# Kernel optimization log

Hardware: AMD Instinct MI355X
Metric: run time of the kernel (lower is better)

Reference implementation:

```python
import jax, jax.numpy as jnp
import numpy as np

N, LQ, C = 1, 12240, 256
HEADS, LEVELS, FRAMES, POINTS = 8, 4, 4, 4
D_HEAD = C // HEADS  # 32
SHAPES = np.array([[48, 48, 4], [24, 24, 4], [12, 12, 4], [6, 6, 4]], np.int32)  # (H, W, T)
LEN_IN = int((SHAPES[:, 0] * SHAPES[:, 1] * SHAPES[:, 2]).sum())  # 12240
assert LEN_IN == LQ


def setup_inputs() -> dict:
    key = jax.random.key(0)
    ks = jax.random.split(key, 9)
    starts = np.concatenate([[0], np.cumsum(SHAPES[:, 0] * SHAPES[:, 1] * SHAPES[:, 2])[:-1]]).astype(np.int32)
    off_dim = HEADS * LEVELS * FRAMES * POINTS * 2
    attn_dim = HEADS * LEVELS * FRAMES * POINTS
    s = 1.0 / np.sqrt(C)
    return {
        "query": jax.random.normal(ks[0], (N, LQ, C), jnp.float32),
        "reference_points": jax.random.uniform(ks[1], (N, LQ, LEVELS, 2), dtype=jnp.float32),
        "temporal_offsets": 0.05 * jax.random.normal(ks[2], (LQ, LEVELS, FRAMES, 2), jnp.float32),
        "input_flatten": jax.random.normal(ks[3], (N, LEN_IN, C), jnp.float32),
        "input_spatial_shapes": jnp.asarray(SHAPES),
        "input_level_start_index": jnp.asarray(starts),
        "W_off": 0.01 * jax.random.normal(ks[4], (C, off_dim), jnp.float32),
        "b_off": 0.1 * jax.random.normal(ks[5], (off_dim,), jnp.float32),
        "W_attn": 0.02 * jax.random.normal(ks[6], (C, attn_dim), jnp.float32),
        "b_attn": jnp.zeros((attn_dim,), jnp.float32),
        "W_val": s * jax.random.normal(ks[7], (C, C), jnp.float32),
        "b_val": jnp.zeros((C,), jnp.float32),
        "W_out": s * jax.random.normal(ks[8], (C, C), jnp.float32),
        "b_out": jnp.zeros((C,), jnp.float32),
    }


def ms_deform_core(value, shapes_hw, starts, loc, attn_w):
    """value: (N, Len_in, Hh, D); loc: (N, Lq, Hh, L, P, 2) in [0,1];
    attn_w: (N, Lq, Hh, L, P); shapes_hw/starts: python ints per level.
    Bilinear sampling matches F.grid_sample(align_corners=False, padding_mode='zeros')."""
    n, _, hh, d = value.shape
    lq, p = loc.shape[1], loc.shape[4]
    out = jnp.zeros((n, hh, lq, d), value.dtype)
    for lid, (hl, wl) in enumerate(shapes_hw):
        s0 = starts[lid]
        v = jnp.transpose(value[:, s0:s0 + hl * wl], (0, 2, 1, 3))  # (N, Hh, H*W, D)
        x = loc[:, :, :, lid, :, 0] * wl - 0.5  # (N, Lq, Hh, P) pixel coords
        y = loc[:, :, :, lid, :, 1] * hl - 0.5
        x0 = jnp.floor(x)
        y0 = jnp.floor(y)
        fx, fy = x - x0, y - y0
        x0i, y0i = x0.astype(jnp.int32), y0.astype(jnp.int32)
        acc = jnp.zeros((n, hh, lq, p, d), value.dtype)
        corners = ((0, 0, (1 - fx) * (1 - fy)), (0, 1, fx * (1 - fy)),
                   (1, 0, (1 - fx) * fy), (1, 1, fx * fy))
        for dy, dx, w in corners:
            xi, yi = x0i + dx, y0i + dy
            valid = (xi >= 0) & (xi < wl) & (yi >= 0) & (yi < hl)
            idx = jnp.clip(yi, 0, hl - 1) * wl + jnp.clip(xi, 0, wl - 1)  # (N, Lq, Hh, P)
            idx_t = jnp.transpose(idx, (0, 2, 1, 3)).reshape(n, hh, lq * p, 1)
            g = jnp.take_along_axis(v, idx_t, axis=2).reshape(n, hh, lq, p, d)
            wm = jnp.transpose(jnp.where(valid, w, 0.0), (0, 2, 1, 3))  # (N, Hh, Lq, P)
            acc = acc + g * wm[..., None]
        aw = jnp.transpose(attn_w[:, :, :, lid], (0, 2, 1, 3))  # (N, Hh, Lq, P)
        out = out + jnp.sum(acc * aw[..., None], axis=3)
    return jnp.transpose(out, (0, 2, 1, 3)).reshape(n, lq, hh * d)


def reference(query, reference_points, temporal_offsets, input_flatten,
              input_spatial_shapes, input_level_start_index,
              W_off, b_off, W_attn, b_attn, W_val, b_val, W_out, b_out):
    shapes = np.asarray(input_spatial_shapes)  # static (L, 3) = (H, W, T)
    starts = [int(s) for s in np.asarray(input_level_start_index)]
    n, lq, _ = query.shape
    value = (input_flatten @ W_val + b_val).reshape(n, -1, HEADS, D_HEAD)
    attn = jax.nn.softmax((query @ W_attn + b_attn)
                          .reshape(n, lq, HEADS, LEVELS * FRAMES * POINTS), axis=-1)
    attn = attn.reshape(n, lq, HEADS, LEVELS, FRAMES * POINTS)
    off = (query @ W_off + b_off).reshape(n, lq, HEADS, LEVELS, FRAMES, POINTS, 2)
    # offset_normalizer = (T, H*W) per level: x spans frames, y spans flattened pixels
    norm = jnp.stack([jnp.asarray(shapes[:, 2], jnp.float32),
                      jnp.asarray(shapes[:, 0] * shapes[:, 1], jnp.float32)], axis=-1)  # (L, 2)
    loc = temporal_offsets[None, :, None, :, :, None, :] + off / norm[None, None, None, :, None, None, :]
    loc = loc.reshape(n, lq, HEADS, LEVELS, FRAMES * POINTS, 2)
    loc = reference_points[:, :, None, :, None, :] + loc
    shapes_hw = [(int(h) * int(w), int(t)) for h, w, t in shapes]  # (H*W, T) grids
    out = ms_deform_core(value, shapes_hw, starts, loc, attn)
    return out @ W_out + b_out
```

## Files before the change

kernel.cpp:

```cpp
#include <hip/hip_runtime.h>
#include <hip/hip_bf16.h>
#include <hip/hip_fp16.h>

#define LQ     12240

typedef _Float16 half8 __attribute__((ext_vector_type(8)));
typedef float floatx4 __attribute__((ext_vector_type(4)));
typedef unsigned int uint;

__global__ __launch_bounds__(256) void cvt_f32_f16(
    const float* __restrict__ in, __half* __restrict__ out, int n4) {
  const int i = blockIdx.x * 256 + threadIdx.x;
  if (i >= n4) return;
  const float4 v = reinterpret_cast<const float4*>(in)[i];
  const __half2 a = __floats2half2_rn(v.x, v.y);
  const __half2 b = __floats2half2_rn(v.z, v.w);
  uint2 pk;
  pk.x = *reinterpret_cast<const uint*>(&a);
  pk.y = *reinterpret_cast<const uint*>(&b);
  reinterpret_cast<uint2*>(out)[i] = pk;
}

__global__ __launch_bounds__(256) void transpose_cvt(
    const float* __restrict__ in, __half* __restrict__ out, int N) {
  __shared__ float t[32][33];
  const int n0 = blockIdx.x * 32, k0 = blockIdx.y * 32;
  const int c = threadIdx.x & 31, r = threadIdx.x >> 5;
#pragma unroll
  for (int i = 0; i < 4; ++i)
    t[r + i * 8][c] = in[(size_t)(k0 + r + i * 8) * N + n0 + c];
  __syncthreads();
#pragma unroll
  for (int i = 0; i < 4; ++i)
    out[(size_t)(n0 + r + i * 8) * 256 + k0 + c] = __float2half(t[c][r + i * 8]);
}

template <typename TC>
__device__ inline void store_c(TC* C, size_t idx, float v);
template <> __device__ inline void store_c<float>(float* C, size_t idx, float v) { C[idx] = v; }
template <> __device__ inline void store_c<__half>(__half* C, size_t idx, float v) { C[idx] = __float2half(v); }

template <typename TC>
__global__ __launch_bounds__(256) void gemm_mfma(
    const __half* __restrict__ A,
    const __half* __restrict__ Bt,
    const float* __restrict__ bias,
    TC* __restrict__ C, int M, int N) {
  __shared__ uint4 As_g[128 * 8];
  __shared__ uint4 Bs_g[128 * 8];

  const int tid = threadIdx.x;
  const int bm = blockIdx.y * 128, bn = blockIdx.x * 128;
  const int wid = tid >> 6, lane = tid & 63;
  const int wr = wid >> 1, wn = wid & 1;
  const int l16 = lane & 15, lhi = lane >> 4;

  floatx4 acc[4][4] = {};

  const int srow = tid >> 1;
  const int sg0 = (tid & 1) * 4;
  const bool arow_ok = (bm + srow) < M;
  const __half* Arow = A + (size_t)(arow_ok ? bm + srow : 0) * 256;
  const __half* Brow = Bt + (size_t)(bn + srow) * 256;

  for (int ks = 0; ks < 4; ++ks) {
    const int k0 = ks * 64;
#pragma unroll
    for (int i = 0; i < 4; ++i) {
      const int g = sg0 + i;
      uint4 av = make_uint4(0, 0, 0, 0);
      if (arow_ok) av = *reinterpret_cast<const uint4*>(Arow + k0 + g * 8);
      As_g[srow * 8 + (g ^ (srow & 7))] = av;
      Bs_g[srow * 8 + (g ^ (srow & 7))] =
          *reinterpret_cast<const uint4*>(Brow + k0 + g * 8);
    }
    __syncthreads();

#pragma unroll
    for (int kk = 0; kk < 2; ++kk) {
      half8 a[4], b[4];
#pragma unroll
      for (int m = 0; m < 4; ++m) {
        const int row = wr * 64 + m * 16 + l16;
        const int g = kk * 4 + lhi;
        union { uint4 u; half8 h; } cv;
        cv.u = As_g[row * 8 + (g ^ (row & 7))];
        a[m] = cv.h;
      }
#pragma unroll
      for (int n = 0; n < 4; ++n) {
        const int row = wn * 64 + n * 16 + l16;
        const int g = kk * 4 + lhi;
        union { uint4 u; half8 h; } cv;
        cv.u = Bs_g[row * 8 + (g ^ (row & 7))];
        b[n] = cv.h;
      }
#pragma unroll
      for (int m = 0; m < 4; ++m)
#pragma unroll
        for (int n = 0; n < 4; ++n)
          acc[m][n] = __builtin_amdgcn_mfma_f32_16x16x32_f16(a[m], b[n], acc[m][n], 0, 0, 0);
    }
    __syncthreads();
  }

#pragma unroll
  for (int m = 0; m < 4; ++m) {
    const int row0 = bm + wr * 64 + m * 16 + lhi * 4;
#pragma unroll
    for (int n = 0; n < 4; ++n) {
      const int col = bn + wn * 64 + n * 16 + l16;
      const float bv = bias[col];
#pragma unroll
      for (int r = 0; r < 4; ++r) {
        const int row = row0 + r;
        if (row < M) store_c<TC>(C, (size_t)row * N + col, acc[m][n][r] + bv);
      }
    }
  }
}

__device__ inline uint hfma2u(uint a, uint b, uint c) {
  const __half2 ah = *reinterpret_cast<const __half2*>(&a);
  const __half2 bh = *reinterpret_cast<const __half2*>(&b);
  const __half2 ch = *reinterpret_cast<const __half2*>(&c);
  const __half2 r = __hfma2(ah, bh, ch);
  return *reinterpret_cast<const uint*>(&r);
}

__device__ inline uint pack_wr(float w, uint row) {
  const __half hw = __float2half(w);
  return ((uint)__half_as_ushort(hw) << 16) | row;
}

__global__ __launch_bounds__(256, 8) void sample_kernel(
    const __half* __restrict__ value,
    const __half* __restrict__ logits,
    const __half* __restrict__ off,
    const float* __restrict__ tempoff,
    const float* __restrict__ refpts,
    __half* __restrict__ msout) {
  const int q0 = blockIdx.x * 2;
  const int tid = threadIdx.x;

  __shared__ __align__(16) uint spk[4096];
  float* slog = reinterpret_cast<float*>(spk);
  __shared__ float sm_m[16], sm_si[16];

#pragma unroll
  for (int k = 0; k < 4; ++k) {
    const int s = tid + k * 256;
    slog[s] = __half2float(logits[(size_t)(q0 + (s >> 9)) * 512 + (s & 511)]);
  }
  __syncthreads();

  {
    const int g = tid >> 4;
    const int j = tid & 15;
    const float* e = &slog[g * 64];
    float m = fmaxf(fmaxf(e[j], e[j + 16]), fmaxf(e[j + 32], e[j + 48]));
#pragma unroll
    for (int mask = 8; mask >= 1; mask >>= 1) m = fmaxf(m, __shfl_xor(m, mask));
    float s = __expf(e[j] - m) + __expf(e[j + 16] - m) +
              __expf(e[j + 32] - m) + __expf(e[j + 48] - m);
#pragma unroll
    for (int mask = 8; mask >= 1; mask >>= 1) s += __shfl_xor(s, mask);
    if (j == 0) { sm_m[g] = m; sm_si[g] = 1.0f / s; }
  }
  __syncthreads();

  const float HWF[4] = {2304.f, 576.f, 144.f, 36.f};
  const float RHW[4] = {1.f / 2304.f, 1.f / 576.f, 1.f / 144.f, 1.f / 36.f};
  const int   S0[4]  = {0, 9216, 11520, 12096};
  const int   HWI[4] = {2304, 576, 144, 36};

  uint4 rec[4];
  int   ridx[4];
  const int h1   = tid & 7;
  const int smid = (tid >> 3) & 7;
  const int shi  = (tid >> 6) & 3;

#pragma unroll
  for (int k = 0; k < 4; ++k) {
    const int qi = k & 1;
    const int s  = smid | (shi << 3) | ((k >> 1) << 5);
    const int i  = h1 * 64 + s;
    const int l  = s >> 4;
    const int f  = (s >> 2) & 3;
    const size_t q = (size_t)(q0 + qi);
    const int g = (qi << 3) | h1;

    const float w = __expf(slog[(qi << 9) + i] - sm_m[g]) * sm_si[g];

    const float2 o  = __half22float2(*reinterpret_cast<const __half2*>(&off[q * 1024 + i * 2]));
    const float2 to = *reinterpret_cast<const float2*>(&tempoff[q * 32 + (l * 4 + f) * 2]);
    const float2 rp = *reinterpret_cast<const float2*>(&refpts[q * 8 + l * 2]);

    const float hw = HWF[l];
    const float x = (to.x + o.x * 0.25f + rp.x) * 4.0f - 0.5f;
    const float y = (to.y + o.y * RHW[l] + rp.y) * hw - 0.5f;

    const float x0f = floorf(x), y0f = floorf(y);
    const float fx = x - x0f, fy = y - y0f;
    const int x0 = (int)x0f, y0 = (int)y0f;
    const int hl = HWI[l];

    const bool xv0 = (x0 >= 0) && (x0 < 4);
    const bool xv1 = (x0 >= -1) && (x0 < 3);
    const bool yv0 = (y0 >= 0) && (y0 < hl);
    const bool yv1 = (y0 >= -1) && (y0 < hl - 1);
    const int xc0 = min(max(x0, 0), 3);
    const int xc1 = min(max(x0 + 1, 0), 3);
    const int yc0 = min(max(y0, 0), hl - 1);
    const int yc1 = min(max(y0 + 1, 0), hl - 1);

    const float w00 = (xv0 && yv0) ? w * (1.f - fx) * (1.f - fy) : 0.f;
    const float w01 = (xv1 && yv0) ? w * fx * (1.f - fy) : 0.f;
    const float w10 = (xv0 && yv1) ? w * (1.f - fx) * fy : 0.f;
    const float w11 = (xv1 && yv1) ? w * fx * fy : 0.f;

    const int base = S0[l];
    rec[k] = make_uint4(pack_wr(w00, (uint)(base + yc0 * 4 + xc0)),
                        pack_wr(w01, (uint)(base + yc0 * 4 + xc1)),
                        pack_wr(w10, (uint)(base + yc1 * 4 + xc0)),
                        pack_wr(w11, (uint)(base + yc1 * 4 + xc1)));
    ridx[k] = (qi << 9) | (s << 3) | h1;
  }
  __syncthreads();

  uint4* spk4 = reinterpret_cast<uint4*>(spk);
#pragma unroll
  for (int k = 0; k < 4; ++k) spk4[ridx[k]] = rec[k];
  __syncthreads();

  const int qi = tid >> 7;
  const int h  = (tid >> 4) & 7;
  const int c  = (tid >> 2) & 3;
  const int d  = tid & 3;

  const uint* __restrict__ sp = spk + ((qi << 11) | (h << 2) | c);
  const char* __restrict__ vbase = (const char*)value + h * 64 + d * 16;

  float f0 = 0.f, f1 = 0.f, f2 = 0.f, f3 = 0.f;
  float f4 = 0.f, f5 = 0.f, f6 = 0.f, f7 = 0.f;

#pragma unroll
  for (int l = 0; l < 4; ++l) {
    uint a0 = 0u, a1 = 0u, a2 = 0u, a3 = 0u;
#pragma unroll
    for (int t = 0; t < 16; ++t) {
      const uint pk = sp[(l * 16 + t) << 5];
      const uint wdup = __builtin_amdgcn_perm(pk, pk, 0x03020302u);
      const uint4 v = *reinterpret_cast<const uint4*>(vbase + ((pk & 0xFFFFu) << 9));
      a0 = hfma2u(wdup, v.x, a0);
      a1 = hfma2u(wdup, v.y, a1);
      a2 = hfma2u(wdup, v.z, a2);
      a3 = hfma2u(wdup, v.w, a3);
    }
    const float2 p0 = __half22float2(*reinterpret_cast<const __half2*>(&a0));
    const float2 p1 = __half22float2(*reinterpret_cast<const __half2*>(&a1));
    const float2 p2 = __half22float2(*reinterpret_cast<const __half2*>(&a2));
    const float2 p3 = __half22float2(*reinterpret_cast<const __half2*>(&a3));
    f0 += p0.x; f1 += p0.y; f2 += p1.x; f3 += p1.y;
    f4 += p2.x; f5 += p2.y; f6 += p3.x; f7 += p3.y;
  }

#pragma unroll
  for (int mask = 4; mask <= 8; mask <<= 1) {
    f0 += __shfl_xor(f0, mask); f1 += __shfl_xor(f1, mask);
    f2 += __shfl_xor(f2, mask); f3 += __shfl_xor(f3, mask);
    f4 += __shfl_xor(f4, mask); f5 += __shfl_xor(f5, mask);
    f6 += __shfl_xor(f6, mask); f7 += __shfl_xor(f7, mask);
  }

  if (c == 0) {
    const __half2 o0 = __floats2half2_rn(f0, f1);
    const __half2 o1 = __floats2half2_rn(f2, f3);
    const __half2 o2 = __floats2half2_rn(f4, f5);
    const __half2 o3 = __floats2half2_rn(f6, f7);
    uint4 st;
    st.x = *reinterpret_cast<const uint*>(&o0);
    st.y = *reinterpret_cast<const uint*>(&o1);
    st.z = *reinterpret_cast<const uint*>(&o2);
    st.w = *reinterpret_cast<const uint*>(&o3);
    *reinterpret_cast<uint4*>(&msout[(size_t)(q0 + qi) * 256 + h * 32 + d * 8]) = st;
  }
}

extern "C" void kernel_launch(void* const* d_in, const int* in_sizes, int n_in,
                              void* d_out, int out_size, void* d_ws, size_t ws_size,
                              hipStream_t stream) {
  const float* query   = (const float*)d_in[0];
  const float* refpts  = (const float*)d_in[1];
  const float* tempoff = (const float*)d_in[2];
  const float* inflat  = (const float*)d_in[3];
  const float* W_off  = (const float*)d_in[6];
  const float* b_off  = (const float*)d_in[7];
  const float* W_attn = (const float*)d_in[8];
  const float* b_attn = (const float*)d_in[9];
  const float* W_val  = (const float*)d_in[10];
  const float* b_val  = (const float*)d_in[11];
  const float* W_out  = (const float*)d_in[12];
  const float* b_out  = (const float*)d_in[13];

  char* ws = (char*)d_ws;
  const size_t szQ = (size_t)LQ * 256 * 2;
  __half* qh     = (__half*)ws;                 ws += szQ;
  __half* ifh    = (__half*)ws;                 ws += szQ;
  __half* wT_val = (__half*)ws;                 ws += (size_t)256 * 256 * 2;
  __half* wT_att = (__half*)ws;                 ws += (size_t)512 * 256 * 2;
  __half* wT_off = (__half*)ws;                 ws += (size_t)1024 * 256 * 2;
  __half* wT_out = (__half*)ws;                 ws += (size_t)256 * 256 * 2;
  __half* val_h  = (__half*)ws;                 ws += szQ;
  __half* attn_h = (__half*)ws;                 ws += (size_t)LQ * 512 * 2;
  __half* off_h  = (__half*)ws;                 ws += (size_t)LQ * 1024 * 2;
  __half* ms_h   = (__half*)ws;                 ws += szQ;

  const dim3 blk(256);
  const int n4 = LQ * 256 / 4;

  cvt_f32_f16<<<dim3((n4 + 255) / 256), blk, 0, stream>>>(query, qh, n4);
  cvt_f32_f16<<<dim3((n4 + 255) / 256), blk, 0, stream>>>(inflat, ifh, n4);
  transpose_cvt<<<dim3(8, 8),  blk, 0, stream>>>(W_val,  wT_val, 256);
  transpose_cvt<<<dim3(16, 8), blk, 0, stream>>>(W_attn, wT_att, 512);
  transpose_cvt<<<dim3(32, 8), blk, 0, stream>>>(W_off,  wT_off, 1024);
  transpose_cvt<<<dim3(8, 8),  blk, 0, stream>>>(W_out,  wT_out, 256);

  const int gm = (LQ + 127) / 128;
  gemm_mfma<__half><<<dim3(2, gm), blk, 0, stream>>>(ifh, wT_val, b_val, val_h, LQ, 256);
  gemm_mfma<__half><<<dim3(4, gm), blk, 0, stream>>>(qh, wT_att, b_attn, attn_h, LQ, 512);
  gemm_mfma<__half><<<dim3(8, gm), blk, 0, stream>>>(qh, wT_off, b_off, off_h, LQ, 1024);

  sample_kernel<<<dim3(LQ / 2), blk, 0, stream>>>(val_h, attn_h, off_h, tempoff, refpts, ms_h);

  gemm_mfma<float><<<dim3(2, gm), blk, 0, stream>>>(ms_h, wT_out, b_out, (float*)d_out, LQ, 256);
}
```

Baseline: 144.3 us.

## Merge prep and projection launches and load GEMM tiles via global_load_lds

The two fp32-to-fp16 conversions become one launch, and the four weight transposes become one launch. The value, attention and offset projection GEMMs merge into a single grid, with the attention and offset weights concatenated into one 1536-wide output that the sampler reads at new offsets. GEMM tile loads now go straight from global memory to LDS with global_load_lds, using a vmcnt wait and scheduling barriers. The aim is to cut launch count and the register round-trip on tile staging. The trade-off is a wider strided output buffer, and the loads are still not double-buffered.

```diff
diff --git a/kernel.cpp b/kernel.cpp
--- a/kernel.cpp
+++ b/kernel.cpp
@@ -8,23 +8,39 @@
 typedef float floatx4 __attribute__((ext_vector_type(4)));
 typedef unsigned int uint;
 
-__global__ __launch_bounds__(256) void cvt_f32_f16(
-    const float* __restrict__ in, __half* __restrict__ out, int n4) {
-  const int i = blockIdx.x * 256 + threadIdx.x;
-  if (i >= n4) return;
+__global__ __launch_bounds__(256) void cvt2_f32_f16(
+    const float* __restrict__ a, const float* __restrict__ b,
+    __half* __restrict__ oa, __half* __restrict__ ob, int n4each) {
+  int i = blockIdx.x * 256 + threadIdx.x;
+  const float* in = a;
+  __half* out = oa;
+  if (i >= n4each) { in = b; out = ob; i -= n4each; }
   const float4 v = reinterpret_cast<const float4*>(in)[i];
-  const __half2 a = __floats2half2_rn(v.x, v.y);
-  const __half2 b = __floats2half2_rn(v.z, v.w);
+  const __half2 p0 = __floats2half2_rn(v.x, v.y);
+  const __half2 p1 = __floats2half2_rn(v.z, v.w);
   uint2 pk;
-  pk.x = *reinterpret_cast<const uint*>(&a);
-  pk.y = *reinterpret_cast<const uint*>(&b);
+  pk.x = *reinterpret_cast<const uint*>(&p0);
+  pk.y = *reinterpret_cast<const uint*>(&p1);
   reinterpret_cast<uint2*>(out)[i] = pk;
 }
 
-__global__ __launch_bounds__(256) void transpose_cvt(
-    const float* __restrict__ in, __half* __restrict__ out, int N) {
+__global__ __launch_bounds__(256) void transpose_all(
+    const float* __restrict__ W_val, const float* __restrict__ W_attn,
+    const float* __restrict__ W_off, const float* __restrict__ W_out,
+    __half* __restrict__ wT_val, __half* __restrict__ wT_ao,
+    __half* __restrict__ wT_out) {
+  int b = blockIdx.x;
+  const float* in;
+  __half* out;
+  int N;
+  if (b < 64) { in = W_val; out = wT_val; N = 256; }
+  else if (b < 192) { b -= 64; in = W_attn; out = wT_ao; N = 512; }
+  else if (b < 448) { b -= 192; in = W_off; out = wT_ao + (size_t)512 * 256; N = 1024; }
+  else { b -= 448; in = W_out; out = wT_out; N = 256; }
+  const int nb = N / 32;
+  const int n0 = (b % nb) * 32, k0 = (b / nb) * 32;
+
   __shared__ float t[32][33];
-  const int n0 = blockIdx.x * 32, k0 = blockIdx.y * 32;
   const int c = threadIdx.x & 31, r = threadIdx.x >> 5;
 #pragma unroll
   for (int i = 0; i < 4; ++i)
@@ -33,6 +49,12 @@
 #pragma unroll
   for (int i = 0; i < 4; ++i)
     out[(size_t)(n0 + r + i * 8) * 256 + k0 + c] = __float2half(t[c][r + i * 8]);
+}
+
+__device__ inline void gl_lds16(const __half* g, void* lds) {
+  __builtin_amdgcn_global_load_lds(
+      (const __attribute__((address_space(1))) void*)g,
+      (__attribute__((address_space(3))) void*)lds, 16, 0, 0);
 }
 
 template <typename TC>
@@ -41,39 +63,40 @@
 template <> __device__ inline void store_c<__half>(__half* C, size_t idx, float v) { C[idx] = __float2half(v); }
 
 template <typename TC>
-__global__ __launch_bounds__(256) void gemm_mfma(
-    const __half* __restrict__ A,
-    const __half* __restrict__ Bt,
-    const float* __restrict__ bias,
-    TC* __restrict__ C, int M, int N) {
-  __shared__ uint4 As_g[128 * 8];
-  __shared__ uint4 Bs_g[128 * 8];
+__device__ inline void gemm_core(
+    const __half* __restrict__ A, const __half* __restrict__ Bt,
+    const float* __restrict__ bias, int coff, TC* __restrict__ C,
+    int M, int N, int bm, int bn) {
+  __shared__ uint4 As_g[1024];
+  __shared__ uint4 Bs_g[1024];
 
   const int tid = threadIdx.x;
-  const int bm = blockIdx.y * 128, bn = blockIdx.x * 128;
-  const int wid = tid >> 6, lane = tid & 63;
-  const int wr = wid >> 1, wn = wid & 1;
+  const int w = tid >> 6, lane = tid & 63;
+  const int wr = w >> 1, wn = w & 1;
   const int l16 = lane & 15, lhi = lane >> 4;
 
   floatx4 acc[4][4] = {};
 
-  const int srow = tid >> 1;
-  const int sg0 = (tid & 1) * 4;
-  const bool arow_ok = (bm + srow) < M;
-  const __half* Arow = A + (size_t)(arow_ok ? bm + srow : 0) * 256;
-  const __half* Brow = Bt + (size_t)(bn + srow) * 256;
+  int srow[4], sgr[4];
+#pragma unroll
+  for (int j = 0; j < 4; ++j) {
+    const int idx = (w * 4 + j) * 64 + lane;
+    srow[j] = idx >> 3;
+    sgr[j] = (idx & 7) ^ (srow[j] & 7);
+  }
 
   for (int ks = 0; ks < 4; ++ks) {
     const int k0 = ks * 64;
 #pragma unroll
-    for (int i = 0; i < 4; ++i) {
-      const int g = sg0 + i;
-      uint4 av = make_uint4(0, 0, 0, 0);
-      if (arow_ok) av = *reinterpret_cast<const uint4*>(Arow + k0 + g * 8);
-      As_g[srow * 8 + (g ^ (srow & 7))] = av;
-      Bs_g[srow * 8 + (g ^ (srow & 7))] =
-          *reinterpret_cast<const uint4*>(Brow + k0 + g * 8);
+    for (int j = 0; j < 4; ++j) {
+      int ar = bm + srow[j];
+      if (ar >= M) ar = M - 1;
+      gl_lds16(A + (size_t)ar * 256 + k0 + sgr[j] * 8, &As_g[(w * 4 + j) * 64]);
+      gl_lds16(Bt + (size_t)(bn + srow[j]) * 256 + k0 + sgr[j] * 8,
+               &Bs_g[(w * 4 + j) * 64]);
     }
+    asm volatile("s_waitcnt vmcnt(0)" ::: "memory");
+    __builtin_amdgcn_sched_barrier(0);
     __syncthreads();
 
 #pragma unroll
@@ -101,7 +124,9 @@
         for (int n = 0; n < 4; ++n)
           acc[m][n] = __builtin_amdgcn_mfma_f32_16x16x32_f16(a[m], b[n], acc[m][n], 0, 0, 0);
     }
+    __builtin_amdgcn_sched_barrier(0);
     __syncthreads();
+    __builtin_amdgcn_sched_barrier(0);
   }
 
 #pragma unroll
@@ -110,7 +135,7 @@
 #pragma unroll
     for (int n = 0; n < 4; ++n) {
       const int col = bn + wn * 64 + n * 16 + l16;
-      const float bv = bias[col];
+      const float bv = bias[col - coff];
 #pragma unroll
       for (int r = 0; r < 4; ++r) {
         const int row = row0 + r;
@@ -118,6 +143,31 @@
       }
     }
   }
+}
+
+__global__ __launch_bounds__(256) void gemm_fused(
+    const __half* __restrict__ qh, const __half* __restrict__ ifh,
+    const __half* __restrict__ wT_val, const __half* __restrict__ wT_ao,
+    const float* __restrict__ b_val, const float* __restrict__ b_attn,
+    const float* __restrict__ b_off,
+    __half* __restrict__ val_h, __half* __restrict__ ao_h, int M) {
+  const int bx = blockIdx.x;
+  const int bm = blockIdx.y * 128;
+  if (bx < 2) {
+    gemm_core<__half>(ifh, wT_val, b_val, 0, val_h, M, 256, bm, bx * 128);
+  } else {
+    const int bn = (bx - 2) * 128;
+    const float* bias = (bn < 512) ? b_attn : b_off;
+    const int coff = (bn < 512) ? 0 : 512;
+    gemm_core<__half>(qh, wT_ao, bias, coff, ao_h, M, 1536, bm, bn);
+  }
+}
+
+__global__ __launch_bounds__(256) void gemm_out_k(
+    const __half* __restrict__ ms_h, const __half* __restrict__ wT_out,
+    const float* __restrict__ b_out, float* __restrict__ C, int M) {
+  gemm_core<float>(ms_h, wT_out, b_out, 0, C, M, 256, blockIdx.y * 128,
+                   blockIdx.x * 128);
 }
 
 __device__ inline uint hfma2u(uint a, uint b, uint c) {
@@ -135,8 +185,7 @@
 
 __global__ __launch_bounds__(256, 8) void sample_kernel(
     const __half* __restrict__ value,
-    const __half* __restrict__ logits,
-    const __half* __restrict__ off,
+    const __half* __restrict__ ao,
     const float* __restrict__ tempoff,
     const float* __restrict__ refpts,
     __half* __restrict__ msout) {
@@ -150,7 +199,7 @@
 #pragma unroll
   for (int k = 0; k < 4; ++k) {
     const int s = tid + k * 256;
-    slog[s] = __half2float(logits[(size_t)(q0 + (s >> 9)) * 512 + (s & 511)]);
+    slog[s] = __half2float(ao[(size_t)(q0 + (s >> 9)) * 1536 + (s & 511)]);
   }
   __syncthreads();
 
@@ -192,7 +241,7 @@
 
     const float w = __expf(slog[(qi << 9) + i] - sm_m[g]) * sm_si[g];
 
-    const float2 o  = __half22float2(*reinterpret_cast<const __half2*>(&off[q * 1024 + i * 2]));
+    const float2 o  = __half22float2(*reinterpret_cast<const __half2*>(&ao[q * 1536 + 512 + i * 2]));
     const float2 to = *reinterpret_cast<const float2*>(&tempoff[q * 32 + (l * 4 + f) * 2]);
     const float2 rp = *reinterpret_cast<const float2*>(&refpts[q * 8 + l * 2]);
 
@@ -308,30 +357,25 @@
   __half* qh     = (__half*)ws;                 ws += szQ;
   __half* ifh    = (__half*)ws;                 ws += szQ;
   __half* wT_val = (__half*)ws;                 ws += (size_t)256 * 256 * 2;
-  __half* wT_att = (__half*)ws;                 ws += (size_t)512 * 256 * 2;
-  __half* wT_off = (__half*)ws;                 ws += (size_t)1024 * 256 * 2;
+  __half* wT_ao  = (__half*)ws;                 ws += (size_t)1536 * 256 * 2;
   __half* wT_out = (__half*)ws;                 ws += (size_t)256 * 256 * 2;
   __half* val_h  = (__half*)ws;                 ws += szQ;
-  __half* attn_h = (__half*)ws;                 ws += (size_t)LQ * 512 * 2;
-  __half* off_h  = (__half*)ws;                 ws += (size_t)LQ * 1024 * 2;
+  __half* ao_h   = (__half*)ws;                 ws += (size_t)LQ * 1536 * 2;
   __half* ms_h   = (__half*)ws;                 ws += szQ;
 
   const dim3 blk(256);
-  const int n4 = LQ * 256 / 4;
-
-  cvt_f32_f16<<<dim3((n4 + 255) / 256), blk, 0, stream>>>(query, qh, n4);
-  cvt_f32_f16<<<dim3((n4 + 255) / 256), blk, 0, stream>>>(inflat, ifh, n4);
-  transpose_cvt<<<dim3(8, 8),  blk, 0, stream>>>(W_val,  wT_val, 256);
-  transpose_cvt<<<dim3(16, 8), blk, 0, stream>>>(W_attn, wT_att, 512);
-  transpose_cvt<<<dim3(32, 8), blk, 0, stream>>>(W_off,  wT_off, 1024);
-  transpose_cvt<<<dim3(8, 8),  blk, 0, stream>>>(W_out,  wT_out, 256);
+  const int n4each = LQ * 256 / 4;
+
+  cvt2_f32_f16<<<dim3(2 * n4each / 256), blk, 0, stream>>>(query, inflat, qh, ifh, n4each);
+  transpose_all<<<dim3(512), blk, 0, stream>>>(W_val, W_attn, W_off, W_out,
+                                               wT_val, wT_ao, wT_out);
 
   const int gm = (LQ + 127) / 128;
-  gemm_mfma<__half><<<dim3(2, gm), blk, 0, stream>>>(ifh, wT_val, b_val, val_h, LQ, 256);
-  gemm_mfma<__half><<<dim3(4, gm), blk, 0, stream>>>(qh, wT_att, b_attn, attn_h, LQ, 512);
-  gemm_mfma<__half><<<dim3(8, gm), blk, 0, stream>>>(qh, wT_off, b_off, off_h, LQ, 1024);
-
-  sample_kernel<<<dim3(LQ / 2), blk, 0, stream>>>(val_h, attn_h, off_h, tempoff, refpts, ms_h);
-
-  gemm_mfma<float><<<dim3(2, gm), blk, 0, stream>>>(ms_h, wT_out, b_out, (float*)d_out, LQ, 256);
-}
+  gemm_fused<<<dim3(14, gm), blk, 0, stream>>>(qh, ifh, wT_val, wT_ao,
+                                               b_val, b_attn, b_off,
+                                               val_h, ao_h, LQ);
+
+  sample_kernel<<<dim3(LQ / 2), blk, 0, stream>>>(val_h, ao_h, tempoff, refpts, ms_h);
+
+  gemm_out_k<<<dim3(2, gm), blk, 0, stream>>>(ms_h, wT_out, b_out, (float*)d_out, LQ);
+}
```

After: 158.3 us. 9.7% more time.
